# Kernel optimization log

Measured on AMD Instinct MI355X. Metric: run time of the kernel, lower is better.

## Reference

```python
import jax, jax.numpy as jnp
import numpy as np

S, B, N, K, D, H = 4, 8, 2048, 16, 32, 128


def setup_inputs() -> dict:
    key = jax.random.key(0)
    ks = jax.random.split(key, 7)
    x = jax.random.normal(ks[0], (S, B, N, D), dtype=jnp.float32)
    mu = jax.random.normal(ks[1], (S, B, K, D), dtype=jnp.float32)
    tau = jax.random.uniform(ks[2], (S, B, K, D), dtype=jnp.float32)  # precisions > 0
    # Linear(3D -> H); stored as (3D, H) i.e. transpose of torch's (H, 3D) weight
    W1 = jax.random.normal(ks[3], (3 * D, H), dtype=jnp.float32) * (1.0 / np.sqrt(3 * D))
    b1 = jax.random.normal(ks[4], (H,), dtype=jnp.float32) * 0.01
    W2 = jax.random.normal(ks[5], (H, 1), dtype=jnp.float32) * (1.0 / np.sqrt(H))
    b2 = jax.random.normal(ks[6], (1,), dtype=jnp.float32) * 0.01
    return {"x": x, "mu": mu, "tau": tau, "W1": W1, "b1": b1, "W2": W2, "b2": b2}


def reference(x, mu, tau, W1, b1, W2, b2):
    # Original torch code materializes var = cat([x_expand, mu_expand, tau_expand], -1)
    # of shape (S,B,N,K,3D) then applies Linear(3D,H). Mathematically identical:
    # split W1 rows into the x / mu / tau blocks and add the partial projections,
    # which avoids building the (S,B,N,K,3D) concat tensor.
    d = x.shape[-1]
    Wx, Wm, Wt = W1[:d], W1[d:2 * d], W1[2 * d:]
    hx = jnp.einsum('sbnd,dh->sbnh', x, Wx)                       # (S,B,N,H)
    hk = jnp.einsum('sbkd,dh->sbkh', mu, Wm) \
       + jnp.einsum('sbkd,dh->sbkh', tau, Wt)                     # (S,B,K,H)
    h = jnp.tanh(hx[:, :, :, None, :] + hk[:, :, None, :, :] + b1)  # (S,B,N,K,H)
    gamma = jnp.einsum('sbnkh,h->sbnk', h, W2[:, 0]) + b2[0]        # (S,B,N,K)
    q_probs = jax.nn.softmax(gamma, axis=-1)
    return q_probs
```

## Files before the change

kernel.cpp:

```cpp
#include <hip/hip_runtime.h>
#include <math.h>

typedef _Float16 half_t;
typedef __attribute__((ext_vector_type(8))) _Float16 half8;

#define EXP2F(x) __builtin_amdgcn_exp2f(x)
#define RCPF(x)  __builtin_amdgcn_rcpf(x)
#define C_SCALE 2.8853900817779268f

__global__ __launch_bounds__(256) void prep_kernel(
    const float* __restrict__ mu, const float* __restrict__ tau,
    const float* __restrict__ W1, const float* __restrict__ b1,
    const float* __restrict__ W2,
    half_t* __restrict__ ek, half_t* __restrict__ w2h) {
  int g = blockIdx.x * 256 + threadIdx.x;
  int h = g & 127, row = g >> 7;
  const float* mur  = mu  + row * 32;
  const float* taur = tau + row * 32;
  float acc = b1[h];
#pragma unroll
  for (int d = 0; d < 32; ++d) {
    acc = fmaf(mur[d],  W1[(32 + d) * 128 + h], acc);
    acc = fmaf(taur[d], W1[(64 + d) * 128 + h], acc);
  }
  ek[g] = (half_t)EXP2F(C_SCALE * acc);
  if (g < 128) w2h[g] = (half_t)(-2.0f * W2[g]);
}

__global__ __launch_bounds__(256, 3) void main_kernel(
    const float* __restrict__ x, const float* __restrict__ W1,
    const half_t* __restrict__ ek, const half_t* __restrict__ w2h,
    float* __restrict__ out) {
  __shared__ __align__(16) float  sX[64][36];
  __shared__ __align__(16) float  sW[32][132];
  __shared__ __align__(16) half_t sEx[64][136];
  __shared__ __align__(16) half_t sEk[16][136];
  __shared__ __align__(16) half_t sW2[128];

  int t = threadIdx.x;
  int row0 = blockIdx.x * 64;
  int sb = row0 >> 11;

  const float4* x4 = (const float4*)(x + (size_t)row0 * 32);
#pragma unroll
  for (int i = 0; i < 2; ++i) {
    int j = i * 256 + t;
    int n = j >> 3, d4 = j & 7;
    *(float4*)&sX[n][d4 * 4] = x4[j];
  }
  const float4* w4 = (const float4*)W1;
#pragma unroll
  for (int i = 0; i < 4; ++i) {
    int j = i * 256 + t;
    int d = j >> 5, h4 = j & 31;
    float4 v = w4[j];
    v.x *= C_SCALE; v.y *= C_SCALE; v.z *= C_SCALE; v.w *= C_SCALE;
    *(float4*)&sW[d][h4 * 4] = v;
  }
  {
    const float4* ek4 = (const float4*)(ek + (size_t)sb * 2048);
    int k = t >> 4, h8 = t & 15;
    *(float4*)&sEk[k][h8 * 8] = ek4[t];
  }
  if (t < 16) *(float4*)&sW2[t * 8] = ((const float4*)w2h)[t];
  __syncthreads();

  {
    int hg = t & 15, rg = t >> 4;
    int h0 = hg * 8, r0 = rg * 4;
    float acc[4][8];
#pragma unroll
    for (int j = 0; j < 4; ++j)
#pragma unroll
      for (int l = 0; l < 8; ++l) acc[j][l] = 0.f;
#pragma unroll 4
    for (int d = 0; d < 32; ++d) {
      float4 wa = *(const float4*)&sW[d][h0];
      float4 wb = *(const float4*)&sW[d][h0 + 4];
      float w[8] = {wa.x, wa.y, wa.z, wa.w, wb.x, wb.y, wb.z, wb.w};
#pragma unroll
      for (int j = 0; j < 4; ++j) {
        float xv = sX[r0 + j][d];
#pragma unroll
        for (int l = 0; l < 8; ++l) acc[j][l] = fmaf(xv, w[l], acc[j][l]);
      }
    }
#pragma unroll
    for (int j = 0; j < 4; ++j) {
      half8 hv;
#pragma unroll
      for (int l = 0; l < 8; ++l) hv[l] = (half_t)EXP2F(acc[j][l]);
      *(half8*)&sEx[r0 + j][h0] = hv;
    }
  }
  __syncthreads();

  int kg = t & 7, rg = t >> 3;
  int r0 = rg * 2, k0 = kg * 2;
  float a00 = 0.f, a01 = 0.f, a10 = 0.f, a11 = 0.f;
#pragma unroll 2
  for (int h8 = 0; h8 < 16; ++h8) {
    half8 ex0 = *(const half8*)&sEx[r0][h8 * 8];
    half8 ex1 = *(const half8*)&sEx[r0 + 1][h8 * 8];
    half8 ekv0 = *(const half8*)&sEk[k0][h8 * 8];
    half8 ekv1 = *(const half8*)&sEk[k0 + 1][h8 * 8];
    half8 wv = *(const half8*)&sW2[h8 * 8];
#pragma unroll
    for (int j = 0; j < 8; ++j) {
      float e0 = (float)ex0[j], e1 = (float)ex1[j];
      float f0 = (float)ekv0[j], f1 = (float)ekv1[j];
      float w = (float)wv[j];
      a00 = fmaf(w, RCPF(fmaf(e0, f0, 1.0f)), a00);
      a01 = fmaf(w, RCPF(fmaf(e0, f1, 1.0f)), a01);
      a10 = fmaf(w, RCPF(fmaf(e1, f0, 1.0f)), a10);
      a11 = fmaf(w, RCPF(fmaf(e1, f1, 1.0f)), a11);
    }
  }

  const float l2e = 1.4426950408889634f;
  {
    float m = fmaxf(a00, a01);
#pragma unroll
    for (int s = 1; s < 8; s <<= 1) m = fmaxf(m, __shfl_xor(m, s, 8));
    float p0 = EXP2F((a00 - m) * l2e), p1 = EXP2F((a01 - m) * l2e);
    float sum = p0 + p1;
#pragma unroll
    for (int s = 1; s < 8; s <<= 1) sum += __shfl_xor(sum, s, 8);
    float inv = RCPF(sum);
    float2 o = make_float2(p0 * inv, p1 * inv);
    *(float2*)&out[(size_t)(row0 + r0) * 16 + k0] = o;
  }
  {
    float m = fmaxf(a10, a11);
#pragma unroll
    for (int s = 1; s < 8; s <<= 1) m = fmaxf(m, __shfl_xor(m, s, 8));
    float p0 = EXP2F((a10 - m) * l2e), p1 = EXP2F((a11 - m) * l2e);
    float sum = p0 + p1;
#pragma unroll
    for (int s = 1; s < 8; s <<= 1) sum += __shfl_xor(sum, s, 8);
    float inv = RCPF(sum);
    float2 o = make_float2(p0 * inv, p1 * inv);
    *(float2*)&out[(size_t)(row0 + r0 + 1) * 16 + k0] = o;
  }
}

extern "C" void kernel_launch(void* const* d_in, const int* in_sizes, int n_in,
                              void* d_out, int out_size, void* d_ws, size_t ws_size,
                              hipStream_t stream) {
  const float* x   = (const float*)d_in[0];
  const float* mu  = (const float*)d_in[1];
  const float* tau = (const float*)d_in[2];
  const float* W1  = (const float*)d_in[3];
  const float* b1  = (const float*)d_in[4];
  const float* W2  = (const float*)d_in[5];
  float* out = (float*)d_out;

  half_t* ek  = (half_t*)d_ws;
  half_t* w2h = ek + 512 * 128;
  (void)in_sizes; (void)n_in; (void)out_size; (void)ws_size;

  prep_kernel<<<256, 256, 0, stream>>>(mu, tau, W1, b1, W2, ek, w2h);
  main_kernel<<<1024, 256, 0, stream>>>(x, W1, ek, w2h, out);
}
```

Before: 92.52 us.

## Switch intermediates to fp32, halve rows per block, alias LDS for occupancy

Moves the exp-activation intermediates and W2 from fp16 to fp32, removing the half/float conversions in the inner reciprocal loop. Each block now covers 32 rows instead of 64, so the grid doubles, and the Ek/W2 buffers reuse the W1 LDS region after a barrier. Launch bounds rise to 4 blocks per CU. The GEMM thread mapping changes to strided h columns, and each thread computes one row and two k outputs. The costs are an extra barrier, W1 staged twice as often across blocks, and more LDS bandwidth from fp32 loads.

```diff
diff --git a/kernel.cpp b/kernel.cpp
--- a/kernel.cpp
+++ b/kernel.cpp
@@ -1,8 +1,5 @@
 #include <hip/hip_runtime.h>
 #include <math.h>
-
-typedef _Float16 half_t;
-typedef __attribute__((ext_vector_type(8))) _Float16 half8;
 
 #define EXP2F(x) __builtin_amdgcn_exp2f(x)
 #define RCPF(x)  __builtin_amdgcn_rcpf(x)
@@ -12,7 +9,7 @@
     const float* __restrict__ mu, const float* __restrict__ tau,
     const float* __restrict__ W1, const float* __restrict__ b1,
     const float* __restrict__ W2,
-    half_t* __restrict__ ek, half_t* __restrict__ w2h) {
+    float* __restrict__ ek, float* __restrict__ w2f) {
   int g = blockIdx.x * 256 + threadIdx.x;
   int h = g & 127, row = g >> 7;
   const float* mur  = mu  + row * 32;
@@ -23,125 +20,117 @@
     acc = fmaf(mur[d],  W1[(32 + d) * 128 + h], acc);
     acc = fmaf(taur[d], W1[(64 + d) * 128 + h], acc);
   }
-  ek[g] = (half_t)EXP2F(C_SCALE * acc);
-  if (g < 128) w2h[g] = (half_t)(-2.0f * W2[g]);
+  ek[g] = EXP2F(C_SCALE * acc);
+  if (g < 128) w2f[g] = -2.0f * W2[g];
 }
 
-__global__ __launch_bounds__(256, 3) void main_kernel(
+__global__ __launch_bounds__(256, 4) void main_kernel(
     const float* __restrict__ x, const float* __restrict__ W1,
-    const half_t* __restrict__ ek, const half_t* __restrict__ w2h,
+    const float* __restrict__ ek, const float* __restrict__ w2f,
     float* __restrict__ out) {
-  __shared__ __align__(16) float  sX[64][36];
-  __shared__ __align__(16) float  sW[32][132];
-  __shared__ __align__(16) half_t sEx[64][136];
-  __shared__ __align__(16) half_t sEk[16][136];
-  __shared__ __align__(16) half_t sW2[128];
+  __shared__ __align__(16) float lds[9600];
+  float* sW  = lds;
+  float* sX  = lds + 4224;
+  float* sEx = lds + 5376;
+  float* sEk = lds;
+  float* sW2 = lds + 2112;
 
   int t = threadIdx.x;
-  int row0 = blockIdx.x * 64;
+  int row0 = blockIdx.x * 32;
   int sb = row0 >> 11;
 
-  const float4* x4 = (const float4*)(x + (size_t)row0 * 32);
-#pragma unroll
-  for (int i = 0; i < 2; ++i) {
-    int j = i * 256 + t;
-    int n = j >> 3, d4 = j & 7;
-    *(float4*)&sX[n][d4 * 4] = x4[j];
-  }
-  const float4* w4 = (const float4*)W1;
-#pragma unroll
-  for (int i = 0; i < 4; ++i) {
-    int j = i * 256 + t;
-    int d = j >> 5, h4 = j & 31;
-    float4 v = w4[j];
-    v.x *= C_SCALE; v.y *= C_SCALE; v.z *= C_SCALE; v.w *= C_SCALE;
-    *(float4*)&sW[d][h4 * 4] = v;
+  const float4* eksb = (const float4*)(ek + (size_t)sb * 2048);
+  float4 ekr0 = eksb[t * 2];
+  float4 ekr1 = eksb[t * 2 + 1];
+  float w2r = (t < 128) ? w2f[t] : 0.f;
+
+  {
+    float4 v = ((const float4*)(x + (size_t)row0 * 32))[t];
+    int n = t >> 3, d4 = t & 7;
+    *(float4*)&sX[n * 36 + d4 * 4] = v;
   }
   {
-    const float4* ek4 = (const float4*)(ek + (size_t)sb * 2048);
-    int k = t >> 4, h8 = t & 15;
-    *(float4*)&sEk[k][h8 * 8] = ek4[t];
-  }
-  if (t < 16) *(float4*)&sW2[t * 8] = ((const float4*)w2h)[t];
-  __syncthreads();
-
-  {
-    int hg = t & 15, rg = t >> 4;
-    int h0 = hg * 8, r0 = rg * 4;
-    float acc[4][8];
+    const float4* w4 = (const float4*)W1;
 #pragma unroll
-    for (int j = 0; j < 4; ++j)
-#pragma unroll
-      for (int l = 0; l < 8; ++l) acc[j][l] = 0.f;
-#pragma unroll 4
-    for (int d = 0; d < 32; ++d) {
-      float4 wa = *(const float4*)&sW[d][h0];
-      float4 wb = *(const float4*)&sW[d][h0 + 4];
-      float w[8] = {wa.x, wa.y, wa.z, wa.w, wb.x, wb.y, wb.z, wb.w};
-#pragma unroll
-      for (int j = 0; j < 4; ++j) {
-        float xv = sX[r0 + j][d];
-#pragma unroll
-        for (int l = 0; l < 8; ++l) acc[j][l] = fmaf(xv, w[l], acc[j][l]);
-      }
-    }
-#pragma unroll
-    for (int j = 0; j < 4; ++j) {
-      half8 hv;
-#pragma unroll
-      for (int l = 0; l < 8; ++l) hv[l] = (half_t)EXP2F(acc[j][l]);
-      *(half8*)&sEx[r0 + j][h0] = hv;
+    for (int i = 0; i < 4; ++i) {
+      int j = i * 256 + t;
+      int d = j >> 5, h4 = j & 31;
+      float4 v = w4[j];
+      v.x *= C_SCALE; v.y *= C_SCALE; v.z *= C_SCALE; v.w *= C_SCALE;
+      *(float4*)&sW[d * 132 + h4 * 4] = v;
     }
   }
   __syncthreads();
 
-  int kg = t & 7, rg = t >> 3;
-  int r0 = rg * 2, k0 = kg * 2;
-  float a00 = 0.f, a01 = 0.f, a10 = 0.f, a11 = 0.f;
-#pragma unroll 2
-  for (int h8 = 0; h8 < 16; ++h8) {
-    half8 ex0 = *(const half8*)&sEx[r0][h8 * 8];
-    half8 ex1 = *(const half8*)&sEx[r0 + 1][h8 * 8];
-    half8 ekv0 = *(const half8*)&sEk[k0][h8 * 8];
-    half8 ekv1 = *(const half8*)&sEk[k0 + 1][h8 * 8];
-    half8 wv = *(const half8*)&sW2[h8 * 8];
+  {
+    int rg = t >> 5, hg = t & 31;
+    int r0 = rg * 4;
+    float acc[4][4] = {{0.f}};
+#pragma unroll 8
+    for (int d = 0; d < 32; ++d) {
+      float wv0 = sW[d * 132 + hg];
+      float wv1 = sW[d * 132 + hg + 32];
+      float wv2 = sW[d * 132 + hg + 64];
+      float wv3 = sW[d * 132 + hg + 96];
 #pragma unroll
-    for (int j = 0; j < 8; ++j) {
-      float e0 = (float)ex0[j], e1 = (float)ex1[j];
-      float f0 = (float)ekv0[j], f1 = (float)ekv1[j];
-      float w = (float)wv[j];
-      a00 = fmaf(w, RCPF(fmaf(e0, f0, 1.0f)), a00);
-      a01 = fmaf(w, RCPF(fmaf(e0, f1, 1.0f)), a01);
-      a10 = fmaf(w, RCPF(fmaf(e1, f0, 1.0f)), a10);
-      a11 = fmaf(w, RCPF(fmaf(e1, f1, 1.0f)), a11);
+      for (int i = 0; i < 4; ++i) {
+        float xv = sX[(r0 + i) * 36 + d];
+        acc[i][0] = fmaf(xv, wv0, acc[i][0]);
+        acc[i][1] = fmaf(xv, wv1, acc[i][1]);
+        acc[i][2] = fmaf(xv, wv2, acc[i][2]);
+        acc[i][3] = fmaf(xv, wv3, acc[i][3]);
+      }
     }
+#pragma unroll
+    for (int i = 0; i < 4; ++i) {
+      sEx[(r0 + i) * 132 + hg]      = EXP2F(acc[i][0]);
+      sEx[(r0 + i) * 132 + hg + 32] = EXP2F(acc[i][1]);
+      sEx[(r0 + i) * 132 + hg + 64] = EXP2F(acc[i][2]);
+      sEx[(r0 + i) * 132 + hg + 96] = EXP2F(acc[i][3]);
+    }
+  }
+  __syncthreads();
+
+  {
+    int kk = t >> 4, col = (t & 15) * 8;
+    *(float4*)&sEk[kk * 132 + col]     = ekr0;
+    *(float4*)&sEk[kk * 132 + col + 4] = ekr1;
+    if (t < 128) sW2[t] = w2r;
+  }
+  __syncthreads();
+
+  int k2 = t & 7, r = t >> 3;
+  int k0 = k2 * 2;
+  const float* exr  = &sEx[r * 132];
+  const float* ekp0 = &sEk[k0 * 132];
+  const float* ekp1 = &sEk[(k0 + 1) * 132];
+  float a0 = 0.f, a1 = 0.f;
+#pragma unroll 4
+  for (int h4 = 0; h4 < 32; ++h4) {
+    float4 e  = *(const float4*)&exr[h4 * 4];
+    float4 f0 = *(const float4*)&ekp0[h4 * 4];
+    float4 f1 = *(const float4*)&ekp1[h4 * 4];
+    float4 w  = *(const float4*)&sW2[h4 * 4];
+    a0 = fmaf(w.x, RCPF(fmaf(e.x, f0.x, 1.f)), a0);
+    a1 = fmaf(w.x, RCPF(fmaf(e.x, f1.x, 1.f)), a1);
+    a0 = fmaf(w.y, RCPF(fmaf(e.y, f0.y, 1.f)), a0);
+    a1 = fmaf(w.y, RCPF(fmaf(e.y, f1.y, 1.f)), a1);
+    a0 = fmaf(w.z, RCPF(fmaf(e.z, f0.z, 1.f)), a0);
+    a1 = fmaf(w.z, RCPF(fmaf(e.z, f1.z, 1.f)), a1);
+    a0 = fmaf(w.w, RCPF(fmaf(e.w, f0.w, 1.f)), a0);
+    a1 = fmaf(w.w, RCPF(fmaf(e.w, f1.w, 1.f)), a1);
   }
 
   const float l2e = 1.4426950408889634f;
-  {
-    float m = fmaxf(a00, a01);
+  float m = fmaxf(a0, a1);
 #pragma unroll
-    for (int s = 1; s < 8; s <<= 1) m = fmaxf(m, __shfl_xor(m, s, 8));
-    float p0 = EXP2F((a00 - m) * l2e), p1 = EXP2F((a01 - m) * l2e);
-    float sum = p0 + p1;
+  for (int s = 1; s < 8; s <<= 1) m = fmaxf(m, __shfl_xor(m, s, 8));
+  float p0 = EXP2F((a0 - m) * l2e), p1 = EXP2F((a1 - m) * l2e);
+  float sum = p0 + p1;
 #pragma unroll
-    for (int s = 1; s < 8; s <<= 1) sum += __shfl_xor(sum, s, 8);
-    float inv = RCPF(sum);
-    float2 o = make_float2(p0 * inv, p1 * inv);
-    *(float2*)&out[(size_t)(row0 + r0) * 16 + k0] = o;
-  }
-  {
-    float m = fmaxf(a10, a11);
-#pragma unroll
-    for (int s = 1; s < 8; s <<= 1) m = fmaxf(m, __shfl_xor(m, s, 8));
-    float p0 = EXP2F((a10 - m) * l2e), p1 = EXP2F((a11 - m) * l2e);
-    float sum = p0 + p1;
-#pragma unroll
-    for (int s = 1; s < 8; s <<= 1) sum += __shfl_xor(sum, s, 8);
-    float inv = RCPF(sum);
-    float2 o = make_float2(p0 * inv, p1 * inv);
-    *(float2*)&out[(size_t)(row0 + r0 + 1) * 16 + k0] = o;
-  }
+  for (int s = 1; s < 8; s <<= 1) sum += __shfl_xor(sum, s, 8);
+  float inv = RCPF(sum);
+  *(float2*)&out[(size_t)(row0 + r) * 16 + k0] = make_float2(p0 * inv, p1 * inv);
 }
 
 extern "C" void kernel_launch(void* const* d_in, const int* in_sizes, int n_in,
@@ -155,10 +144,10 @@
   const float* W2  = (const float*)d_in[5];
   float* out = (float*)d_out;
 
-  half_t* ek  = (half_t*)d_ws;
-  half_t* w2h = ek + 512 * 128;
+  float* ek  = (float*)d_ws;
+  float* w2f = ek + 512 * 128;
   (void)in_sizes; (void)n_in; (void)out_size; (void)ws_size;
 
-  prep_kernel<<<256, 256, 0, stream>>>(mu, tau, W1, b1, W2, ek, w2h);
-  main_kernel<<<1024, 256, 0, stream>>>(x, W1, ek, w2h, out);
+  prep_kernel<<<256, 256, 0, stream>>>(mu, tau, W1, b1, W2, ek, w2f);
+  main_kernel<<<2048, 256, 0, stream>>>(x, W1, ek, w2f, out);
 }
```

Result: slower. 94.91 us (+2.6%).
